# Kernel tuning notes

Measured on AMD Instinct MI355X. Metric: run time of the kernel, lower is better.

Reference implementation:

```python
import jax, jax.numpy as jnp
import numpy as np

EPS = 1e-5
N_SEGMENT = 8


def _bn(x, g, b, m, v):
    # x: (nt, c) or (nt, c, h, w); params: (c,)
    shape = (1, -1) + (1,) * (x.ndim - 2)
    scale = (g * jax.lax.rsqrt(v + EPS)).reshape(shape)
    return (x - m.reshape(shape)) * scale + b.reshape(shape)


def setup_inputs() -> dict:
    key = jax.random.key(0)
    ks = jax.random.split(key, 20)
    c, c8 = 256, 32
    nt, h, w = 128, 28, 28
    inp = {
        'x': jax.random.normal(ks[0], (nt, c, h, w), jnp.float32),
        'wq': jax.random.normal(ks[1], (c8, c), jnp.float32) * 0.05,
        'bq': jax.random.normal(ks[2], (c8,), jnp.float32) * 0.05,
        'gq': jax.random.uniform(ks[3], (c8,), jnp.float32),
        'betaq': jax.random.normal(ks[4], (c8,), jnp.float32) * 0.05,
        'mq': jax.random.normal(ks[5], (c8,), jnp.float32) * 0.05,
        'vq': jax.random.uniform(ks[6], (c8,), jnp.float32),
        'wk': jax.random.normal(ks[7], (c8, c), jnp.float32) * 0.05,
        'bk': jax.random.normal(ks[8], (c8,), jnp.float32) * 0.05,
        'gk': jax.random.uniform(ks[9], (c8,), jnp.float32),
        'betak': jax.random.normal(ks[10], (c8,), jnp.float32) * 0.05,
        'mk': jax.random.normal(ks[11], (c8,), jnp.float32) * 0.05,
        'vk': jax.random.uniform(ks[12], (c8,), jnp.float32),
        'wi': jax.random.normal(ks[13], (c, c8), jnp.float32) * 0.05,
        'bi': jax.random.normal(ks[14], (c,), jnp.float32) * 0.05,
        'gi': jax.random.uniform(ks[15], (c,), jnp.float32),
        'betai': jax.random.normal(ks[16], (c,), jnp.float32) * 0.05,
        'mi': jax.random.normal(ks[17], (c,), jnp.float32) * 0.05,
        'vi': jax.random.uniform(ks[18], (c,), jnp.float32),
    }
    return inp


def reference(x, wq, bq, gq, betaq, mq, vq, wk, bk, gk, betak, mk, vk,
              wi, bi, gi, betai, mi, vi):
    nt, c, h, w = x.shape
    T = N_SEGMENT
    nb = nt // T
    # conv1x1 + BN(eval) + ReLU, then global avg pool -> (nt, c//n_div)
    q = jnp.einsum('nchw,oc->nohw', x, wq) + bq[None, :, None, None]
    q = jax.nn.relu(_bn(q, gq, betaq, mq, vq)).mean(axis=(2, 3))
    k = jnp.einsum('nchw,oc->nohw', x, wk) + bk[None, :, None, None]
    k = jax.nn.relu(_bn(k, gk, betak, mk, vk)).mean(axis=(2, 3))
    # Trans_att(out_q, out_q, out_v): q and k branches are BOTH q; v is k branch
    q3 = q.reshape(nb, T, -1)
    v3 = k.reshape(nb, T, -1)
    att = -jnp.einsum('bic,bjc->bij', q3, q3)  # (nb, T, T)
    att = jax.nn.softmax(att, axis=1)          # softmax over dim 1 as in torch
    q_upd = jnp.einsum('bij,bjc->bic', att, v3) + v3  # (nb, T, c8)
    q_upd = q_upd.reshape(nt, -1)
    # conv_inflate (1x1 conv on (nt, c8, 1, 1)) + BN + ReLU
    y = q_upd @ wi.T + bi
    y = jax.nn.relu(_bn(y, gi, betai, mi, vi))
    gate = jax.nn.sigmoid(y)                    # (nt, c)
    return gate[:, :, None, None] * x
```

## Files before the change

### kernel.cpp

```cpp
#include <hip/hip_runtime.h>
#include <cstdint>
#include <cstddef>

#define EPSV 1e-5f
typedef uint32_t u32;
typedef unsigned short u16;
typedef __attribute__((ext_vector_type(8))) short bf16x8;
typedef __attribute__((ext_vector_type(4))) float f32x4;

__device__ __forceinline__ u16 f2b(float x){ union { float f; u32 i; } v; v.f=x; u32 t=v.i; return (u16)((t + 0x7fffu + ((t>>16)&1u))>>16); }

__global__ __launch_bounds__(256) void k_prep(
    const float* __restrict__ wq, const float* __restrict__ bq, const float* __restrict__ gq,
    const float* __restrict__ betaq, const float* __restrict__ mq, const float* __restrict__ vq,
    const float* __restrict__ wk, const float* __restrict__ bk, const float* __restrict__ gk,
    const float* __restrict__ betak, const float* __restrict__ mk, const float* __restrict__ vk,
    u16* __restrict__ Wswz, float* __restrict__ D)
{
  const int idx = blockIdx.x*256 + threadIdx.x;
  const int j = idx & 7, lane = (idx >> 3) & 63, nt = (idx >> 9) & 3, kk = idx >> 11;
  const int c = kk*32 + ((lane >> 4) << 3) + j;
  const int o = nt*16 + (lane & 15);
  float w, g, v;
  if (o < 32) { w = wq[o*256 + c];      g = gq[o];    v = vq[o]; }
  else        { w = wk[(o-32)*256 + c]; g = gk[o-32]; v = vk[o-32]; }
  Wswz[idx] = f2b(w * (g * rsqrtf(v + EPSV)));
  if (idx < 64) {
    float gg,b,be,m,vv;
    if (idx < 32) { gg=gq[idx];    b=bq[idx];    be=betaq[idx];    m=mq[idx];    vv=vq[idx]; }
    else          { gg=gk[idx-32]; b=bk[idx-32]; be=betak[idx-32]; m=mk[idx-32]; vv=vk[idx-32]; }
    const float s = gg * rsqrtf(vv + EPSV);
    D[idx] = (b - m)*s + be;
  }
}

__global__ __launch_bounds__(256) void k_stageA(
    const float* __restrict__ x, const u16* __restrict__ Wswz, const float* __restrict__ D,
    float* __restrict__ qk_part)
{
  __shared__ __align__(16) u16 Wl[16384];
  const int tid = threadIdx.x;
  const int n = blockIdx.x / 13, g = blockIdx.x % 13;

  {
    const uint4* src = (const uint4*)Wswz;
    uint4* dst = (uint4*)Wl;
#pragma unroll
    for (int i = 0; i < 8; ++i) dst[tid + i*256] = src[tid + i*256];
  }
  __syncthreads();

  const int wv = tid >> 6, lane = tid & 63;
  const int tile = g*4 + wv;
  const bool active = (tile < 49);

  float s4[4] = {0.f, 0.f, 0.f, 0.f};
  if (active) {
    const int px = tile*16 + (lane & 15);
    const float* xr = x + (size_t)n*200704 + px;
    const int krow = (lane >> 4) * 8;
    const bf16x8* Wf = (const bf16x8*)Wl;

    f32x4 acc[4];
#pragma unroll
    for (int nt = 0; nt < 4; ++nt) acc[nt] = (f32x4){0.f, 0.f, 0.f, 0.f};

    float a[8], an[8];
#pragma unroll
    for (int j = 0; j < 8; ++j) a[j] = xr[(size_t)(krow + j)*784];

#pragma unroll
    for (int kk = 0; kk < 8; ++kk) {
      if (kk < 7) {
#pragma unroll
        for (int j = 0; j < 8; ++j) an[j] = xr[(size_t)((kk+1)*32 + krow + j)*784];
      }
      bf16x8 af;
#pragma unroll
      for (int j = 0; j < 8; ++j) af[j] = (short)f2b(a[j]);
#pragma unroll
      for (int nt = 0; nt < 4; ++nt) {
        const bf16x8 bf = Wf[(kk*4 + nt)*64 + lane];
        acc[nt] = __builtin_amdgcn_mfma_f32_16x16x32_bf16(af, bf, acc[nt], 0, 0, 0);
      }
#pragma unroll
      for (int j = 0; j < 8; ++j) a[j] = an[j];
    }

#pragma unroll
    for (int nt = 0; nt < 4; ++nt) {
      const float d = D[nt*16 + (lane & 15)];
      float s = 0.f;
#pragma unroll
      for (int r = 0; r < 4; ++r) s += fmaxf(acc[nt][r] + d, 0.f);
      s += __shfl_down(s, 16, 64);
      s += __shfl_down(s, 32, 64);
      s4[nt] = s;
    }
  }

  __syncthreads();
  float* red = reinterpret_cast<float*>(Wl);
  if (lane < 16) {
#pragma unroll
    for (int nt = 0; nt < 4; ++nt)
      red[wv*64 + nt*16 + lane] = active ? s4[nt] : 0.f;
  }
  __syncthreads();
  if (tid < 64) {
    qk_part[(size_t)(n*13 + g)*64 + tid] =
        red[tid] + red[64+tid] + red[128+tid] + red[192+tid];
  }
}

__global__ __launch_bounds__(256) void k_stageB(
    const float* __restrict__ qk_part,
    const float* __restrict__ wi, const float* __restrict__ bi, const float* __restrict__ gi,
    const float* __restrict__ betai, const float* __restrict__ mi, const float* __restrict__ vi,
    float* __restrict__ gate)
{
  __shared__ float ql[8][32], vl[8][32], attl[8][8], qul[8][32];
  const int tid = threadIdx.x;
  const int b = blockIdx.x;

  {
    const int i = tid >> 5, c = tid & 31;
    const int n = b*8 + i;
    float sq = 0.f, sv = 0.f;
#pragma unroll
    for (int qq = 0; qq < 13; ++qq) {
      sq += qk_part[(size_t)(n*13 + qq)*64 + c];
      sv += qk_part[(size_t)(n*13 + qq)*64 + 32 + c];
    }
    ql[i][c] = sq * (1.f/784.f);
    vl[i][c] = sv * (1.f/784.f);
  }
  __syncthreads();

  if (tid < 64) {
    const int i = tid >> 3, j = tid & 7;
    float d = 0.f;
#pragma unroll
    for (int c = 0; c < 32; ++c) d += ql[i][c]*ql[j][c];
    float a = -d;
    float m = a;
    m = fmaxf(m, __shfl_xor(m, 8, 64));
    m = fmaxf(m, __shfl_xor(m, 16, 64));
    m = fmaxf(m, __shfl_xor(m, 32, 64));
    const float e = __expf(a - m);
    float s = e;
    s += __shfl_xor(s, 8, 64);
    s += __shfl_xor(s, 16, 64);
    s += __shfl_xor(s, 32, 64);
    attl[i][j] = e / s;
  }
  __syncthreads();

  {
    const int i = tid >> 5, c = tid & 31;
    float acc = vl[i][c];
#pragma unroll
    for (int j = 0; j < 8; ++j) acc = fmaf(attl[i][j], vl[j][c], acc);
    qul[i][c] = acc;
  }
  __syncthreads();

  {
    const int cout = tid;
    float w[32];
#pragma unroll
    for (int k = 0; k < 32; ++k) w[k] = wi[cout*32 + k];
    const float s  = gi[cout] * rsqrtf(vi[cout] + EPSV);
    const float dd = (bi[cout] - mi[cout]) * s + betai[cout];
#pragma unroll
    for (int i = 0; i < 8; ++i) {
      float y = 0.f;
#pragma unroll
      for (int k = 0; k < 32; ++k) y = fmaf(qul[i][k], w[k], y);
      const float t = fmaxf(fmaf(y, s, dd), 0.f);
      gate[(size_t)(b*8 + i)*256 + cout] = 1.f / (1.f + __expf(-t));
    }
  }
}

__global__ __launch_bounds__(256) void k_gateMul(
    const float* __restrict__ x, const float* __restrict__ gate, float* __restrict__ out)
{
  const u32 nchunk = 128u*256u*196u;
  const u32 stride = gridDim.x * 256u;
  for (u32 q = blockIdx.x*256u + threadIdx.x; q < nchunk; q += stride) {
    const u32 cn = q / 196u;
    const float g = gate[cn];
    const float4 v = reinterpret_cast<const float4*>(x)[q];
    float4 o4;
    o4.x = v.x * g; o4.y = v.y * g; o4.z = v.z * g; o4.w = v.w * g;
    reinterpret_cast<float4*>(out)[q] = o4;
  }
}

extern "C" void kernel_launch(void* const* d_in, const int* in_sizes, int n_in,
                              void* d_out, int out_size, void* d_ws, size_t ws_size,
                              hipStream_t stream) {
  const float* x    = (const float*)d_in[0];
  const float* wq   = (const float*)d_in[1];
  const float* bq   = (const float*)d_in[2];
  const float* gq   = (const float*)d_in[3];
  const float* betaq= (const float*)d_in[4];
  const float* mq   = (const float*)d_in[5];
  const float* vq   = (const float*)d_in[6];
  const float* wk   = (const float*)d_in[7];
  const float* bk   = (const float*)d_in[8];
  const float* gk   = (const float*)d_in[9];
  const float* betak= (const float*)d_in[10];
  const float* mk   = (const float*)d_in[11];
  const float* vk   = (const float*)d_in[12];
  const float* wi   = (const float*)d_in[13];
  const float* bi   = (const float*)d_in[14];
  const float* gi   = (const float*)d_in[15];
  const float* betai= (const float*)d_in[16];
  const float* mi   = (const float*)d_in[17];
  const float* vi   = (const float*)d_in[18];

  char* ws = (char*)d_ws;
  float* qk_part = (float*)(ws);
  float* gate    = (float*)(ws + 425984);
  u16*   Wswz    = (u16*)  (ws + 557056);
  float* Dc      = (float*)(ws + 589824);

  k_prep<<<64, 256, 0, stream>>>(wq,bq,gq,betaq,mq,vq, wk,bk,gk,betak,mk,vk, Wswz, Dc);
  k_stageA<<<1664, 256, 0, stream>>>(x, Wswz, Dc, qk_part);
  k_stageB<<<16, 256, 0, stream>>>(qk_part, wi,bi,gi,betai,mi,vi, gate);
  k_gateMul<<<2048, 256, 0, stream>>>(x, gate, (float*)d_out);
}
```

Before: 66.87 us.

## Fuse weight prep into stage A and use nontemporal stores in gate multiply

Removes the separate k_prep launch: each stage A block now folds the BN scale into the conv weights itself, converts them to bf16 and writes them straight into LDS, with the bias terms kept in shared memory. The first x loads are issued before the weight staging so their latency overlaps it. The gate multiply now writes its output with nontemporal stores. The cost is that every one of the 1664 blocks repeats the weight folding and reads the raw fp32 weights, which are likely served from cache.

```diff
diff --git a/kernel.cpp b/kernel.cpp
--- a/kernel.cpp
+++ b/kernel.cpp
@@ -10,65 +10,69 @@
 
 __device__ __forceinline__ u16 f2b(float x){ union { float f; u32 i; } v; v.f=x; u32 t=v.i; return (u16)((t + 0x7fffu + ((t>>16)&1u))>>16); }
 
-__global__ __launch_bounds__(256) void k_prep(
+__global__ __launch_bounds__(256) void k_stageA(
+    const float* __restrict__ x,
     const float* __restrict__ wq, const float* __restrict__ bq, const float* __restrict__ gq,
     const float* __restrict__ betaq, const float* __restrict__ mq, const float* __restrict__ vq,
     const float* __restrict__ wk, const float* __restrict__ bk, const float* __restrict__ gk,
     const float* __restrict__ betak, const float* __restrict__ mk, const float* __restrict__ vk,
-    u16* __restrict__ Wswz, float* __restrict__ D)
-{
-  const int idx = blockIdx.x*256 + threadIdx.x;
-  const int j = idx & 7, lane = (idx >> 3) & 63, nt = (idx >> 9) & 3, kk = idx >> 11;
-  const int c = kk*32 + ((lane >> 4) << 3) + j;
-  const int o = nt*16 + (lane & 15);
-  float w, g, v;
-  if (o < 32) { w = wq[o*256 + c];      g = gq[o];    v = vq[o]; }
-  else        { w = wk[(o-32)*256 + c]; g = gk[o-32]; v = vk[o-32]; }
-  Wswz[idx] = f2b(w * (g * rsqrtf(v + EPSV)));
-  if (idx < 64) {
-    float gg,b,be,m,vv;
-    if (idx < 32) { gg=gq[idx];    b=bq[idx];    be=betaq[idx];    m=mq[idx];    vv=vq[idx]; }
-    else          { gg=gk[idx-32]; b=bk[idx-32]; be=betak[idx-32]; m=mk[idx-32]; vv=vk[idx-32]; }
-    const float s = gg * rsqrtf(vv + EPSV);
-    D[idx] = (b - m)*s + be;
-  }
-}
-
-__global__ __launch_bounds__(256) void k_stageA(
-    const float* __restrict__ x, const u16* __restrict__ Wswz, const float* __restrict__ D,
     float* __restrict__ qk_part)
 {
   __shared__ __align__(16) u16 Wl[16384];
+  __shared__ float Dsh[64];
   const int tid = threadIdx.x;
   const int n = blockIdx.x / 13, g = blockIdx.x % 13;
-
-  {
-    const uint4* src = (const uint4*)Wswz;
-    uint4* dst = (uint4*)Wl;
-#pragma unroll
-    for (int i = 0; i < 8; ++i) dst[tid + i*256] = src[tid + i*256];
-  }
-  __syncthreads();
-
   const int wv = tid >> 6, lane = tid & 63;
   const int tile = g*4 + wv;
   const bool active = (tile < 49);
 
+  const int px = tile*16 + (lane & 15);
+  const float* xr = x + (size_t)n*200704 + px;
+  const int krow = (lane >> 4) * 8;
+  float a[8];
+  if (active) {
+#pragma unroll
+    for (int j = 0; j < 8; ++j) a[j] = xr[(size_t)(krow + j)*784];
+  }
+
+#pragma unroll
+  for (int k8 = 0; k8 < 8; ++k8) {
+    const int f = tid + k8*256;
+    const int fl = f & 63, nt = (f >> 6) & 3, kk = f >> 8;
+    const int c0 = kk*32 + ((fl >> 4) << 3);
+    const int o = nt*16 + (fl & 15);
+    const float* wrow; float gg, vv;
+    if (o < 32) { wrow = wq + o*256 + c0;      gg = gq[o];    vv = vq[o]; }
+    else        { wrow = wk + (o-32)*256 + c0; gg = gk[o-32]; vv = vk[o-32]; }
+    const float s = gg * rsqrtf(vv + EPSV);
+    u32 p[4];
+#pragma unroll
+    for (int h = 0; h < 4; ++h) {
+      const u32 lo = f2b(wrow[2*h] * s);
+      const u32 hi = f2b(wrow[2*h+1] * s);
+      p[h] = lo | (hi << 16);
+    }
+    uint4 pk; pk.x = p[0]; pk.y = p[1]; pk.z = p[2]; pk.w = p[3];
+    reinterpret_cast<uint4*>(Wl)[f] = pk;
+  }
+  if (tid < 64) {
+    const int o = tid;
+    float gg,b,be,m,vv;
+    if (o < 32) { gg=gq[o];    b=bq[o];    be=betaq[o];    m=mq[o];    vv=vq[o]; }
+    else        { gg=gk[o-32]; b=bk[o-32]; be=betak[o-32]; m=mk[o-32]; vv=vk[o-32]; }
+    const float s = gg * rsqrtf(vv + EPSV);
+    Dsh[o] = (b - m)*s + be;
+  }
+  __syncthreads();
+
   float s4[4] = {0.f, 0.f, 0.f, 0.f};
   if (active) {
-    const int px = tile*16 + (lane & 15);
-    const float* xr = x + (size_t)n*200704 + px;
-    const int krow = (lane >> 4) * 8;
     const bf16x8* Wf = (const bf16x8*)Wl;
-
     f32x4 acc[4];
 #pragma unroll
     for (int nt = 0; nt < 4; ++nt) acc[nt] = (f32x4){0.f, 0.f, 0.f, 0.f};
 
-    float a[8], an[8];
-#pragma unroll
-    for (int j = 0; j < 8; ++j) a[j] = xr[(size_t)(krow + j)*784];
-
+    float an[8];
 #pragma unroll
     for (int kk = 0; kk < 8; ++kk) {
       if (kk < 7) {
@@ -89,7 +93,7 @@
 
 #pragma unroll
     for (int nt = 0; nt < 4; ++nt) {
-      const float d = D[nt*16 + (lane & 15)];
+      const float d = Dsh[nt*16 + (lane & 15)];
       float s = 0.f;
 #pragma unroll
       for (int r = 0; r < 4; ++r) s += fmaxf(acc[nt][r] + d, 0.f);
@@ -191,10 +195,9 @@
   for (u32 q = blockIdx.x*256u + threadIdx.x; q < nchunk; q += stride) {
     const u32 cn = q / 196u;
     const float g = gate[cn];
-    const float4 v = reinterpret_cast<const float4*>(x)[q];
-    float4 o4;
-    o4.x = v.x * g; o4.y = v.y * g; o4.z = v.z * g; o4.w = v.w * g;
-    reinterpret_cast<float4*>(out)[q] = o4;
+    const f32x4 v = reinterpret_cast<const f32x4*>(x)[q];
+    const f32x4 o4 = v * g;
+    __builtin_nontemporal_store(o4, reinterpret_cast<f32x4*>(out) + q);
   }
 }
 
@@ -224,11 +227,8 @@
   char* ws = (char*)d_ws;
   float* qk_part = (float*)(ws);
   float* gate    = (float*)(ws + 425984);
-  u16*   Wswz    = (u16*)  (ws + 557056);
-  float* Dc      = (float*)(ws + 589824);
-
-  k_prep<<<64, 256, 0, stream>>>(wq,bq,gq,betaq,mq,vq, wk,bk,gk,betak,mk,vk, Wswz, Dc);
-  k_stageA<<<1664, 256, 0, stream>>>(x, Wswz, Dc, qk_part);
+
+  k_stageA<<<1664, 256, 0, stream>>>(x, wq,bq,gq,betaq,mq,vq, wk,bk,gk,betak,mk,vk, qk_part);
   k_stageB<<<16, 256, 0, stream>>>(qk_part, wi,bi,gi,betai,mi,vi, gate);
   k_gateMul<<<2048, 256, 0, stream>>>(x, gate, (float*)d_out);
 }
```

Result: slower. 71.49 us (+6.9%).
